# Kernel tuning notes

Measured on AMD Instinct MI355X. Metric: run time of the kernel, lower is better.

The kernel has to match this reference:

```python
import jax, jax.numpy as jnp
import numpy as np

B, H, W, DIM = 32, 56, 56, 192
WSZ = 7
HEADS = 8
DK = 32
DV = 32
INNER_K = HEADS * DK  # 256
INNER_V = HEADS * DV  # 256


def setup_inputs() -> dict:
    key = jax.random.key(0)
    ks = jax.random.split(key, 8)
    s = 0.05
    return {
        "x": jax.random.normal(ks[0], (B, H, W, DIM), jnp.float32),
        "Wq": jax.random.normal(ks[1], (DIM, INNER_K), jnp.float32) * s,
        "Wk": jax.random.normal(ks[2], (DIM, INNER_K), jnp.float32) * s,
        "Wv": jax.random.normal(ks[3], (DIM, INNER_V), jnp.float32) * s,
        "Wlocal": jax.random.normal(ks[4], (3, 3, INNER_V, INNER_V), jnp.float32) * s,
        "b_local": jnp.zeros((INNER_V,), jnp.float32),
        "Wout": jax.random.normal(ks[5], (INNER_V, DIM), jnp.float32) * s,
        "b_out": jnp.zeros((DIM,), jnp.float32),
    }


def _window(t, heads, wsz):
    # (b, H, W, heads*d) -> (b*nx*ny, heads, wsz*wsz, d)
    b, h, w, c = t.shape
    d = c // heads
    nx, ny = h // wsz, w // wsz
    t = t.reshape(b, nx, wsz, ny, wsz, heads, d)
    t = t.transpose(0, 1, 3, 5, 2, 4, 6)
    return t.reshape(b * nx * ny, heads, wsz * wsz, d)


def reference(x, Wq, Wk, Wv, Wlocal, b_local, Wout, b_out):
    scale = DK ** (-0.5)
    # 1x1 convs == per-pixel matmuls
    q = jnp.einsum('bhwc,cd->bhwd', x, Wq)
    k = jnp.einsum('bhwc,cd->bhwd', x, Wk)
    v = jnp.einsum('bhwc,cd->bhwd', x, Wv)
    # 3x3 local interactive conv on v (SAME padding)
    local_out = jax.lax.conv_general_dilated(
        v, Wlocal, window_strides=(1, 1), padding='SAME',
        dimension_numbers=('NHWC', 'HWIO', 'NHWC')) + b_local
    # window partition
    qw = _window(q, HEADS, WSZ)
    kw = _window(k, HEADS, WSZ)
    vw = _window(v, HEADS, WSZ)
    dots = jnp.einsum('bhid,bhjd->bhij', qw, kw) * scale  # (B*nx*ny, heads, 49, 49)
    attn = jax.nn.softmax(dots, axis=-1)
    out = jnp.einsum('bhij,bhjd->bhid', attn, vw)
    # window merge: (b*nx*ny, heads, wsz*wsz, d) -> (b, H, W, heads*d)
    nx, ny = H // WSZ, W // WSZ
    out = out.reshape(B, nx, ny, HEADS, WSZ, WSZ, DV)
    out = out.transpose(0, 1, 4, 2, 5, 3, 6).reshape(B, H, W, HEADS * DV)
    out = out + local_out
    out = jnp.einsum('bhwc,cd->bhwd', out, Wout) + b_out
    return out
```

## Files before the change

### kernel.cpp

```cpp
#include <hip/hip_runtime.h>

typedef unsigned short ushort_t;
typedef __bf16  bf16x8 __attribute__((ext_vector_type(8)));
typedef float   f32x4  __attribute__((ext_vector_type(4)));
typedef unsigned short u16x8 __attribute__((ext_vector_type(8)));

#define MFMA16(a,b,c) __builtin_amdgcn_mfma_f32_16x16x32_bf16((a),(b),(c),0,0,0)
#define WAITVM(N) asm volatile("s_waitcnt vmcnt(" #N ")" ::: "memory")
#define BARRIER() do{ __builtin_amdgcn_s_barrier(); asm volatile("" ::: "memory"); }while(0)

static __device__ __forceinline__ ushort_t f2bf(float f){
  __bf16 h = (__bf16)f;
  return __builtin_bit_cast(ushort_t, h);
}
static __device__ __forceinline__ float bf2f(ushort_t b){
  union{unsigned u; float f;} x; x.u = ((unsigned)b)<<16; return x.f;
}
static __device__ __forceinline__ bf16x8 ldg_bf8u(const ushort_t* p){
  u16x8 r = *(const u16x8*)p;
  return __builtin_bit_cast(bf16x8, r);
}
static __device__ __forceinline__ bf16x8 lds_bf8(const ushort_t* p){
  u16x8 r = *(const u16x8*)p;
  return __builtin_bit_cast(bf16x8, r);
}
static __device__ __forceinline__ void gload_lds16(const ushort_t* g, ushort_t* l){
  __builtin_amdgcn_global_load_lds(
      (const __attribute__((address_space(1))) void*)g,
      (__attribute__((address_space(3))) void*)l, 16, 0, 0);
}

__global__ __launch_bounds__(256) void prep_kernel(
    const float* __restrict__ Wq, const float* __restrict__ Wk,
    const float* __restrict__ Wv, const float* __restrict__ Wl,
    const float* __restrict__ Wo,
    ushort_t* __restrict__ qkvT, ushort_t* __restrict__ wlT,
    ushort_t* __restrict__ woT)
{
  int idx = blockIdx.x*256 + threadIdx.x;
  if(idx < 147456){
    int n = idx/192, kk = idx%192;
    const float* W = (n < 256) ? Wq : ((n < 512) ? Wk : Wv);
    qkvT[idx] = f2bf(W[kk*256 + (n & 255)]);
  } else if(idx < 147456 + 589824){
    int t2 = idx - 147456;
    int j   = t2 & 7;
    int sl  = (t2 >> 3) & 3;
    int col = (t2 >> 5) & 255;
    int ks  = (t2 >> 13) & 7;
    int tap = t2 >> 16;
    int grp = sl ^ ((col>>1)&3);
    int k = ks*32 + grp*8 + j;
    wlT[t2] = f2bf(Wl[((size_t)tap*256 + k)*256 + col]);
  } else if(idx < 737280 + 49152){
    int t3 = idx - 737280;
    int col = t3/256, kk = t3%256;
    woT[t3] = f2bf(Wo[kk*192 + col]);
  }
}

__global__ __launch_bounds__(512,2) void qkvattn_kernel(
    const float* __restrict__ x, const ushort_t* __restrict__ WT,
    ushort_t* __restrict__ vbuf, ushort_t* __restrict__ attnout)
{
  __shared__ ushort_t lds[53248];
  ushort_t* xLds = lds;
  const int tid = threadIdx.x;
  const int w = tid>>6, l = tid&63, lr = l&15, g = l>>4;
  const int win = blockIdx.x;
  const int b = win>>6, rem = win&63, wy = rem>>3, wx = rem&7;
  const size_t base = (size_t)b*3136 + wy*7*56 + wx*7;

  #pragma unroll
  for(int r=0;r<3;++r){
    int c = tid + r*512;
    int row = c/24, cp = c%24;
    if(row < 49){
      int sc = cp ^ (row&7);
      const float* src = x + (base + (row/7)*56 + (row%7))*192 + sc*8;
      float4 f0 = *(const float4*)src;
      float4 f1 = *(const float4*)(src+4);
      u16x8 o;
      o[0]=f2bf(f0.x); o[1]=f2bf(f0.y); o[2]=f2bf(f0.z); o[3]=f2bf(f0.w);
      o[4]=f2bf(f1.x); o[5]=f2bf(f1.y); o[6]=f2bf(f1.z); o[7]=f2bf(f1.w);
      *(u16x8*)&xLds[row*192 + cp*8] = o;
    } else {
      u16x8 z = {0,0,0,0,0,0,0,0};
      *(u16x8*)&xLds[row*192 + cp*8] = z;
    }
  }
  __syncthreads();

  ushort_t* qkBase = lds + 16384 + w*4608;
  ushort_t* vT     = lds + w*2048;
  const ushort_t* Wq_ = WT + (size_t)(w*32)*192;
  const ushort_t* Wk_ = WT + (size_t)(256 + w*32)*192;
  const ushort_t* Wv_ = WT + (size_t)(512 + w*32)*192;
  f32x4 aq[4][2], ak[4][2], av[4][2];
  #pragma unroll
  for(int mi=0;mi<4;++mi)
    #pragma unroll
    for(int nj=0;nj<2;++nj){
      f32x4 z={0.f,0.f,0.f,0.f};
      aq[mi][nj]=z; ak[mi][nj]=z; av[mi][nj]=z;
    }
  #pragma unroll
  for(int ks=0; ks<6; ++ks){
    bf16x8 af[4];
    #pragma unroll
    for(int mi=0;mi<4;++mi){
      int row = mi*16 + lr;
      af[mi] = lds_bf8(&xLds[(row*192 + ks*32 + g*8) ^ ((row&7)<<3)]);
    }
    bf16x8 bq[2], bk[2], bv[2];
    #pragma unroll
    for(int nj=0;nj<2;++nj){
      size_t off = (size_t)(nj*16+lr)*192 + ks*32 + g*8;
      bq[nj] = ldg_bf8u(Wq_ + off);
      bk[nj] = ldg_bf8u(Wk_ + off);
      bv[nj] = ldg_bf8u(Wv_ + off);
    }
    #pragma unroll
    for(int nj=0;nj<2;++nj)
      #pragma unroll
      for(int mi=0;mi<4;++mi){
        aq[mi][nj] = MFMA16(af[mi], bq[nj], aq[mi][nj]);
        ak[mi][nj] = MFMA16(af[mi], bk[nj], ak[mi][nj]);
        av[mi][nj] = MFMA16(af[mi], bv[nj], av[mi][nj]);
      }
  }
  #pragma unroll
  for(int mi=0;mi<4;++mi)
    #pragma unroll
    for(int nj=0;nj<2;++nj)
      #pragma unroll
      for(int i=0;i<4;++i){
        int row = mi*16 + g*4 + i, col = nj*16 + lr;
        qkBase[row*36 + col]        = f2bf(aq[mi][nj][i]);
        qkBase[2304 + row*36 + col] = f2bf(ak[mi][nj][i]);
      }
  __syncthreads();
  #pragma unroll
  for(int mi=0;mi<4;++mi)
    #pragma unroll
    for(int nj=0;nj<2;++nj)
      #pragma unroll
      for(int i=0;i<4;++i){
        int row = mi*16 + g*4 + i, col = nj*16 + lr;
        ushort_t val = f2bf(av[mi][nj][i]);
        vT[(col*64 + row) ^ ((col&7)<<3)] = val;
        if(row < 49)
          vbuf[(base + (row/7)*56 + (row%7))*256 + w*32 + col] = val;
      }

  f32x4 dot[4][4];
  #pragma unroll
  for(int mi=0;mi<4;++mi)
    #pragma unroll
    for(int nj=0;nj<4;++nj){ f32x4 z={0.f,0.f,0.f,0.f}; dot[mi][nj]=z; }
  bf16x8 qf[4], kf[4];
  #pragma unroll
  for(int t=0;t<4;++t){
    qf[t] = lds_bf8(&qkBase[(t*16+lr)*36 + g*8]);
    kf[t] = lds_bf8(&qkBase[2304 + (t*16+lr)*36 + g*8]);
  }
  #pragma unroll
  for(int mi=0;mi<4;++mi)
    #pragma unroll
    for(int nj=0;nj<4;++nj)
      dot[mi][nj] = MFMA16(qf[mi], kf[nj], dot[mi][nj]);

  const float sc = 0.17677669529663687f * 1.4426950408889634f;
  ushort_t* pl = qkBase;
  #pragma unroll
  for(int mi=0;mi<4;++mi)
    #pragma unroll
    for(int nj=0;nj<4;++nj){
      int col = nj*16 + lr;
      #pragma unroll
      for(int i=0;i<4;++i){
        float e = (col < 49) ? exp2f(dot[mi][nj][i]*sc) : 0.f;
        int row = mi*16 + g*4 + i;
        pl[(row*64 + col) ^ ((row&7)<<3)] = f2bf(e);
      }
    }

  u16x8 ones_u = {0x3f80,0x3f80,0x3f80,0x3f80,0x3f80,0x3f80,0x3f80,0x3f80};
  bf16x8 ones8 = __builtin_bit_cast(bf16x8, ones_u);
  f32x4 o[4][2], rsum[4];
  #pragma unroll
  for(int mi=0;mi<4;++mi){
    f32x4 z={0.f,0.f,0.f,0.f};
    o[mi][0]=z; o[mi][1]=z; rsum[mi]=z;
  }
  #pragma unroll
  for(int ks=0;ks<2;++ks){
    bf16x8 pa[4];
    #pragma unroll
    for(int mi=0;mi<4;++mi){
      int row = mi*16 + lr;
      pa[mi] = lds_bf8(&pl[(row*64 + ks*32 + g*8) ^ ((row&7)<<3)]);
    }
    #pragma unroll
    for(int nj=0;nj<2;++nj){
      int d = nj*16 + lr;
      bf16x8 vb = lds_bf8(&vT[(d*64 + ks*32 + g*8) ^ ((d&7)<<3)]);
      #pragma unroll
      for(int mi=0;mi<4;++mi) o[mi][nj] = MFMA16(pa[mi], vb, o[mi][nj]);
    }
    #pragma unroll
    for(int mi=0;mi<4;++mi) rsum[mi] = MFMA16(pa[mi], ones8, rsum[mi]);
  }
  #pragma unroll
  for(int mi=0;mi<4;++mi){
    #pragma unroll
    for(int i=0;i<4;++i){
      int row = mi*16 + g*4 + i;
      if(row < 49){
        size_t pix = base + (row/7)*56 + (row%7);
        float inv = 1.0f / rsum[mi][i];
        #pragma unroll
        for(int nj=0;nj<2;++nj)
          attnout[pix*256 + w*32 + nj*16 + lr] = f2bf(o[mi][nj][i] * inv);
      }
    }
  }
}

__global__ __launch_bounds__(256,2) void conv_kernel(
    const ushort_t* __restrict__ v, const ushort_t* __restrict__ WlT,
    const float* __restrict__ b_local, ushort_t* __restrict__ local_out)
{
  __shared__ ushort_t aBuf[2][256*32];
  __shared__ ushort_t bBuf[3][256*32];
  const int bid = blockIdx.x;
  const int tile = (bid & 7) * 98 + (bid >> 3);
  const int p0 = tile * 128;
  const int tid = threadIdx.x;
  const int l = tid&63, w=tid>>6, wm=w>>1, wn=w&1, lr=l&15, g=l>>4;

  unsigned maskbits[4];
  int pxloc[4];
  #pragma unroll
  for(int mi=0;mi<4;++mi){
    int p = p0 + wm*64 + mi*16 + lr;
    int rem = p % 3136;
    int y = rem/56, x = rem%56;
    unsigned mb = 0;
    #pragma unroll
    for(int tap=0;tap<9;++tap){
      int dy = tap/3 - 1, dx = tap%3 - 1;
      if(((unsigned)(y+dy) < 56u) && ((unsigned)(x+dx) < 56u)) mb |= (1u<<tap);
    }
    maskbits[mi] = mb;
    pxloc[mi] = wm*64 + mi*16 + lr + 64;
  }

  auto stageA = [&](int ks, ushort_t* dst){
    #pragma unroll
    for(int r=0;r<4;++r){
      int c = tid + r*256;
      int px = c>>2, sl = c&3;
      int px_abs = p0 - 64 + px;
      px_abs = min(max(px_abs, 0), 100351);
      int chunk = sl ^ ((px>>1)&3);
      gload_lds16(v + (size_t)px_abs*256 + ks*32 + chunk*8,
                  dst + (size_t)(r*256 + w*64)*8);
    }
  };
  auto stageB = [&](int ks, int tap, ushort_t* dst){
    const ushort_t* src = WlT + ((size_t)tap*8 + ks)*8192;
    #pragma unroll
    for(int r=0;r<4;++r){
      gload_lds16(src + (size_t)(tid + r*256)*8,
                  dst + (size_t)(r*256 + w*64)*8);
    }
  };

  f32x4 acc[4][8];
  #pragma unroll
  for(int mi=0;mi<4;++mi)
    #pragma unroll
    for(int nj=0;nj<8;++nj){ f32x4 z={0.f,0.f,0.f,0.f}; acc[mi][nj]=z; }

  auto compute = [&](int tap, const ushort_t* aL, const ushort_t* bL){
    int shift = (tap/3 - 1)*56 + (tap%3 - 1);
    bf16x8 af[4];
    #pragma unroll
    for(int mi=0;mi<4;++mi){
      int px = pxloc[mi] + shift;
      int sl = g ^ ((px>>1)&3);
      u16x8 rv = *(const u16x8*)&aL[px*32 + sl*8];
      if(!((maskbits[mi]>>tap)&1)){ u16x8 z={0,0,0,0,0,0,0,0}; rv=z; }
      af[mi] = __builtin_bit_cast(bf16x8, rv);
    }
    __builtin_amdgcn_s_setprio(1);
    #pragma unroll
    for(int nj=0;nj<8;++nj){
      int col = wn*128 + nj*16 + lr;
      int slb = g ^ ((col>>1)&3);
      bf16x8 bfr = lds_bf8(&bL[col*32 + slb*8]);
      #pragma unroll
      for(int mi=0;mi<4;++mi) acc[mi][nj] = MFMA16(af[mi], bfr, acc[mi][nj]);
    }
    __builtin_amdgcn_s_setprio(0);
  };

  stageA(0, aBuf[0]);
  stageB(0, 0, bBuf[0]);
  stageB(0, 1, bBuf[1]);

  for(int ks=0; ks<7; ++ks){
    #pragma unroll
    for(int tap=0; tap<9; ++tap){
      if(tap==1) WAITVM(8); else WAITVM(4);
      BARRIER();
      if(tap==0) stageA(ks+1, aBuf[(ks+1)&1]);
      stageB(ks + (tap+2)/9, (tap+2)%9, bBuf[(tap+2)%3]);
      compute(tap, aBuf[ks&1], bBuf[tap%3]);
    }
  }
  #pragma unroll
  for(int tap=0; tap<9; ++tap){
    if(tap==8) WAITVM(0); else WAITVM(4);
    BARRIER();
    if(tap<7) stageB(7, tap+2, bBuf[(tap+2)%3]);
    compute(tap, aBuf[1], bBuf[tap%3]);
  }

  #pragma unroll
  for(int nj=0;nj<8;++nj){
    int col = wn*128 + nj*16 + lr;
    float bb = b_local[col];
    #pragma unroll
    for(int mi=0;mi<4;++mi)
      #pragma unroll
      for(int i=0;i<4;++i){
        int p = p0 + wm*64 + mi*16 + g*4 + i;
        local_out[(size_t)p*256 + col] = f2bf(acc[mi][nj][i] + bb);
      }
  }
}

__global__ __launch_bounds__(256,4) void outproj_kernel(
    const ushort_t* __restrict__ attnout, const ushort_t* __restrict__ locl,
    const ushort_t* __restrict__ WoT, const float* __restrict__ b_out,
    float* __restrict__ out)
{
  __shared__ ushort_t aLds[64*256];
  const int m0 = blockIdx.x * 64;
  const int tid = threadIdx.x;
  const int l = tid&63, w = tid>>6, lr=l&15, g=l>>4;
  #pragma unroll
  for(int r=0;r<8;++r){
    int c = tid + r*256;
    int row = c>>5, cc = c&31;
    size_t off = (size_t)(m0+row)*256 + cc*8;
    u16x8 a = *(const u16x8*)(attnout + off);
    u16x8 b2 = *(const u16x8*)(locl + off);
    u16x8 o;
    #pragma unroll
    for(int j=0;j<8;++j) o[j] = f2bf(bf2f(a[j]) + bf2f(b2[j]));
    *(u16x8*)&aLds[(row*256 + cc*8) ^ ((row&7)<<3)] = o;
  }
  __syncthreads();

  const ushort_t* Wbase = WoT + (size_t)(w*48)*256;
  f32x4 acc[4][3];
  #pragma unroll
  for(int mi=0;mi<4;++mi)
    #pragma unroll
    for(int nj=0;nj<3;++nj){ f32x4 z={0.f,0.f,0.f,0.f}; acc[mi][nj]=z; }

  #pragma unroll
  for(int ks=0;ks<8;++ks){
    bf16x8 bfr[3];
    #pragma unroll
    for(int nj=0;nj<3;++nj)
      bfr[nj] = ldg_bf8u(Wbase + (size_t)(nj*16+lr)*256 + ks*32 + g*8);
    bf16x8 af[4];
    #pragma unroll
    for(int mi=0;mi<4;++mi){
      int row = mi*16 + lr;
      af[mi] = lds_bf8(&aLds[(row*256 + ks*32 + g*8) ^ ((row&7)<<3)]);
    }
    #pragma unroll
    for(int nj=0;nj<3;++nj)
      #pragma unroll
      for(int mi=0;mi<4;++mi) acc[mi][nj] = MFMA16(af[mi], bfr[nj], acc[mi][nj]);
  }
  #pragma unroll
  for(int nj=0;nj<3;++nj){
    int col = w*48 + nj*16 + lr;
    float bb = b_out[col];
    #pragma unroll
    for(int mi=0;mi<4;++mi)
      #pragma unroll
      for(int i=0;i<4;++i){
        int row = mi*16 + g*4 + i;
        out[(size_t)(m0+row)*192 + col] = acc[mi][nj][i] + bb;
      }
  }
}

extern "C" void kernel_launch(void* const* d_in, const int* in_sizes, int n_in,
                              void* d_out, int out_size, void* d_ws, size_t ws_size,
                              hipStream_t stream)
{
  const float* x  = (const float*)d_in[0];
  const float* Wq = (const float*)d_in[1];
  const float* Wk = (const float*)d_in[2];
  const float* Wv = (const float*)d_in[3];
  const float* Wl = (const float*)d_in[4];
  const float* bl = (const float*)d_in[5];
  const float* Wo = (const float*)d_in[6];
  const float* bo = (const float*)d_in[7];
  float* out = (float*)d_out;
  char* ws = (char*)d_ws;
  ushort_t* attnout = (ushort_t*)(ws);
  ushort_t* vbuf    = (ushort_t*)(ws + 102760448);
  ushort_t* locl    = (ushort_t*)(ws + 205520896);
  ushort_t* qkvT    = (ushort_t*)(ws + 256901120);
  ushort_t* wlT     = (ushort_t*)(ws + 257196032);
  ushort_t* woT     = (ushort_t*)(ws + 258375680);

  prep_kernel<<<3072, 256, 0, stream>>>(Wq, Wk, Wv, Wl, Wo, qkvT, wlT, woT);
  qkvattn_kernel<<<2048, 512, 0, stream>>>(x, qkvT, vbuf, attnout);
  conv_kernel<<<784, 256, 0, stream>>>(vbuf, wlT, bl, locl);
  outproj_kernel<<<1568, 256, 0, stream>>>(attnout, locl, woT, bo, out);
}
```

Before: 328.8 us.

## Split each attention window across two 256-thread blocks of four heads

The fused QKV-projection and window-attention kernel now launches two blocks per window, each with four waves handling four heads, instead of one 512-thread block covering all eight heads. Shared memory per block drops, so more blocks can be resident per CU. The Q/K projection and the V projection run as separate phases so fewer accumulators are live at once, which lowers register pressure. In exchange, each window's input tile is loaded from global memory and converted to bf16 twice, once per block.

```diff
diff --git a/kernel.cpp b/kernel.cpp
--- a/kernel.cpp
+++ b/kernel.cpp
@@ -59,21 +59,22 @@
   }
 }
 
-__global__ __launch_bounds__(512,2) void qkvattn_kernel(
+__global__ __launch_bounds__(256,2) void qkvattn_kernel(
     const float* __restrict__ x, const ushort_t* __restrict__ WT,
     ushort_t* __restrict__ vbuf, ushort_t* __restrict__ attnout)
 {
-  __shared__ ushort_t lds[53248];
+  __shared__ ushort_t lds[38912];
   ushort_t* xLds = lds;
   const int tid = threadIdx.x;
   const int w = tid>>6, l = tid&63, lr = l&15, g = l>>4;
-  const int win = blockIdx.x;
+  const int bid = blockIdx.x;
+  const int win = bid>>1, head = (bid&1)*4 + w;
   const int b = win>>6, rem = win&63, wy = rem>>3, wx = rem&7;
   const size_t base = (size_t)b*3136 + wy*7*56 + wx*7;
 
   #pragma unroll
-  for(int r=0;r<3;++r){
-    int c = tid + r*512;
+  for(int r=0;r<6;++r){
+    int c = tid + r*256;
     int row = c/24, cp = c%24;
     if(row < 49){
       int sc = cp ^ (row&7);
@@ -91,67 +92,93 @@
   }
   __syncthreads();
 
-  ushort_t* qkBase = lds + 16384 + w*4608;
-  ushort_t* vT     = lds + w*2048;
-  const ushort_t* Wq_ = WT + (size_t)(w*32)*192;
-  const ushort_t* Wk_ = WT + (size_t)(256 + w*32)*192;
-  const ushort_t* Wv_ = WT + (size_t)(512 + w*32)*192;
-  f32x4 aq[4][2], ak[4][2], av[4][2];
-  #pragma unroll
-  for(int mi=0;mi<4;++mi)
-    #pragma unroll
-    for(int nj=0;nj<2;++nj){
-      f32x4 z={0.f,0.f,0.f,0.f};
-      aq[mi][nj]=z; ak[mi][nj]=z; av[mi][nj]=z;
-    }
-  #pragma unroll
-  for(int ks=0; ks<6; ++ks){
-    bf16x8 af[4];
-    #pragma unroll
-    for(int mi=0;mi<4;++mi){
-      int row = mi*16 + lr;
-      af[mi] = lds_bf8(&xLds[(row*192 + ks*32 + g*8) ^ ((row&7)<<3)]);
-    }
-    bf16x8 bq[2], bk[2], bv[2];
-    #pragma unroll
-    for(int nj=0;nj<2;++nj){
-      size_t off = (size_t)(nj*16+lr)*192 + ks*32 + g*8;
-      bq[nj] = ldg_bf8u(Wq_ + off);
-      bk[nj] = ldg_bf8u(Wk_ + off);
-      bv[nj] = ldg_bf8u(Wv_ + off);
-    }
-    #pragma unroll
-    for(int nj=0;nj<2;++nj)
+  ushort_t* qkBase = lds + 12288 + w*4608;
+  ushort_t* vT     = lds + 30720 + w*2048;
+  const ushort_t* Wq_ = WT + (size_t)(head*32)*192;
+  const ushort_t* Wk_ = WT + (size_t)(256 + head*32)*192;
+  const ushort_t* Wv_ = WT + (size_t)(512 + head*32)*192;
+
+  {
+    f32x4 aq[4][2], ak[4][2];
+    #pragma unroll
+    for(int mi=0;mi<4;++mi)
+      #pragma unroll
+      for(int nj=0;nj<2;++nj){
+        f32x4 z={0.f,0.f,0.f,0.f};
+        aq[mi][nj]=z; ak[mi][nj]=z;
+      }
+    #pragma unroll
+    for(int ks=0; ks<6; ++ks){
+      bf16x8 af[4];
       #pragma unroll
       for(int mi=0;mi<4;++mi){
-        aq[mi][nj] = MFMA16(af[mi], bq[nj], aq[mi][nj]);
-        ak[mi][nj] = MFMA16(af[mi], bk[nj], ak[mi][nj]);
-        av[mi][nj] = MFMA16(af[mi], bv[nj], av[mi][nj]);
-      }
-  }
-  #pragma unroll
-  for(int mi=0;mi<4;++mi)
-    #pragma unroll
-    for(int nj=0;nj<2;++nj)
-      #pragma unroll
-      for(int i=0;i<4;++i){
-        int row = mi*16 + g*4 + i, col = nj*16 + lr;
-        qkBase[row*36 + col]        = f2bf(aq[mi][nj][i]);
-        qkBase[2304 + row*36 + col] = f2bf(ak[mi][nj][i]);
-      }
-  __syncthreads();
-  #pragma unroll
-  for(int mi=0;mi<4;++mi)
-    #pragma unroll
-    for(int nj=0;nj<2;++nj)
-      #pragma unroll
-      for(int i=0;i<4;++i){
-        int row = mi*16 + g*4 + i, col = nj*16 + lr;
-        ushort_t val = f2bf(av[mi][nj][i]);
-        vT[(col*64 + row) ^ ((col&7)<<3)] = val;
-        if(row < 49)
-          vbuf[(base + (row/7)*56 + (row%7))*256 + w*32 + col] = val;
-      }
+        int row = mi*16 + lr;
+        af[mi] = lds_bf8(&xLds[(row*192 + ks*32 + g*8) ^ ((row&7)<<3)]);
+      }
+      bf16x8 bq[2], bk[2];
+      #pragma unroll
+      for(int nj=0;nj<2;++nj){
+        size_t off = (size_t)(nj*16+lr)*192 + ks*32 + g*8;
+        bq[nj] = ldg_bf8u(Wq_ + off);
+        bk[nj] = ldg_bf8u(Wk_ + off);
+      }
+      #pragma unroll
+      for(int nj=0;nj<2;++nj)
+        #pragma unroll
+        for(int mi=0;mi<4;++mi){
+          aq[mi][nj] = MFMA16(af[mi], bq[nj], aq[mi][nj]);
+          ak[mi][nj] = MFMA16(af[mi], bk[nj], ak[mi][nj]);
+        }
+    }
+    #pragma unroll
+    for(int mi=0;mi<4;++mi)
+      #pragma unroll
+      for(int nj=0;nj<2;++nj)
+        #pragma unroll
+        for(int i=0;i<4;++i){
+          int row = mi*16 + g*4 + i, col = nj*16 + lr;
+          qkBase[row*36 + col]        = f2bf(aq[mi][nj][i]);
+          qkBase[2304 + row*36 + col] = f2bf(ak[mi][nj][i]);
+        }
+  }
+
+  {
+    f32x4 av[4][2];
+    #pragma unroll
+    for(int mi=0;mi<4;++mi)
+      #pragma unroll
+      for(int nj=0;nj<2;++nj){ f32x4 z={0.f,0.f,0.f,0.f}; av[mi][nj]=z; }
+    #pragma unroll
+    for(int ks=0; ks<6; ++ks){
+      bf16x8 af[4];
+      #pragma unroll
+      for(int mi=0;mi<4;++mi){
+        int row = mi*16 + lr;
+        af[mi] = lds_bf8(&xLds[(row*192 + ks*32 + g*8) ^ ((row&7)<<3)]);
+      }
+      bf16x8 bv[2];
+      #pragma unroll
+      for(int nj=0;nj<2;++nj)
+        bv[nj] = ldg_bf8u(Wv_ + (size_t)(nj*16+lr)*192 + ks*32 + g*8);
+      #pragma unroll
+      for(int nj=0;nj<2;++nj)
+        #pragma unroll
+        for(int mi=0;mi<4;++mi)
+          av[mi][nj] = MFMA16(af[mi], bv[nj], av[mi][nj]);
+    }
+    #pragma unroll
+    for(int mi=0;mi<4;++mi)
+      #pragma unroll
+      for(int nj=0;nj<2;++nj)
+        #pragma unroll
+        for(int i=0;i<4;++i){
+          int row = mi*16 + g*4 + i, col = nj*16 + lr;
+          ushort_t val = f2bf(av[mi][nj][i]);
+          vT[(col*64 + row) ^ ((col&7)<<3)] = val;
+          if(row < 49)
+            vbuf[(base + (row/7)*56 + (row%7))*256 + head*32 + col] = val;
+        }
+  }
 
   f32x4 dot[4][4];
   #pragma unroll
@@ -221,7 +248,7 @@
         float inv = 1.0f / rsum[mi][i];
         #pragma unroll
         for(int nj=0;nj<2;++nj)
-          attnout[pix*256 + w*32 + nj*16 + lr] = f2bf(o[mi][nj][i] * inv);
+          attnout[pix*256 + head*32 + nj*16 + lr] = f2bf(o[mi][nj][i] * inv);
       }
     }
   }
@@ -425,7 +452,7 @@
   ushort_t* woT     = (ushort_t*)(ws + 258375680);
 
   prep_kernel<<<3072, 256, 0, stream>>>(Wq, Wk, Wv, Wl, Wo, qkvT, wlT, woT);
-  qkvattn_kernel<<<2048, 512, 0, stream>>>(x, qkvT, vbuf, attnout);
+  qkvattn_kernel<<<4096, 256, 0, stream>>>(x, qkvT, vbuf, attnout);
   conv_kernel<<<784, 256, 0, stream>>>(vbuf, wlT, bl, locl);
   outproj_kernel<<<1568, 256, 0, stream>>>(attnout, locl, woT, bo, out);
 }
```

After: 323.5 us. Within noise of the previous version (-1.6%).
